# Optimization experiments

Hardware: AMD Instinct MI355X
Metric: run time of the kernel (lower is better)

Reference implementation:

```python
import jax, jax.numpy as jnp
import numpy as np

G, P, F, K = 256, 512, 4, 6   # graphs, nodes/graph, features, knn k
N = G * P

def _prelu(x, a):
    return jnp.where(x >= 0, x, a * x)

def _knn_edges(x):
    # per-graph brute-force kNN (k=6, no self loops), flow source->target
    xg = x.reshape(G, P, F)
    sq = jnp.sum(xg * xg, -1)                                   # [G,P]
    d = sq[:, :, None] + sq[:, None, :] - 2.0 * jnp.einsum('gpf,gqf->gpq', xg, xg)
    d = d + jnp.eye(P, dtype=x.dtype) * 1e10                    # exclude self
    _, idx = jax.lax.top_k(-d, K)                               # [G,P,K] neighbors
    off = (jnp.arange(G) * P)[:, None, None]
    src = (idx + off).reshape(-1)                               # message sources
    tgt = jnp.broadcast_to(jnp.arange(N).reshape(G, P, 1), (G, P, K)).reshape(-1)
    return src, tgt

def setup_inputs():
    key = jax.random.key(0)
    ks = jax.random.split(key, 8)
    f = lambda k, s: jax.random.normal(k, s, jnp.float32) * 0.1
    return {
        "x": jax.random.normal(ks[0], (N, F), jnp.float32),
        "batch": jnp.arange(N, dtype=jnp.int32) // P,
        "pre_W1": f(ks[1], (F, F)), "pre_b1": jnp.zeros((F,), jnp.float32),
        "pre_a1": jnp.full((F,), 0.25, jnp.float32),
        "pre_W2": f(ks[2], (F, F)), "pre_b2": jnp.zeros((F,), jnp.float32),
        "pre_a2": jnp.full((F,), 0.25, jnp.float32),
        "bn_g": jnp.ones((F,), jnp.float32), "bn_b": jnp.zeros((F,), jnp.float32),
        "act_a": jnp.full((F,), 0.25, jnp.float32),
        "conv_Wm": f(ks[3], (4, F, F)), "conv_bm": jnp.zeros((4, F), jnp.float32),
        "hlv_W1": f(ks[4], (5 * F, 5 * F)), "hlv_b1": jnp.zeros((5 * F,), jnp.float32),
        "hlv_W2": f(ks[5], (5 * F, 1)), "hlv_b2": jnp.zeros((1,), jnp.float32),
    }

def reference(x, batch, pre_W1, pre_b1, pre_a1, pre_W2, pre_b2, pre_a2,
              bn_g, bn_b, act_a, conv_Wm, conv_bm, hlv_W1, hlv_b1, hlv_W2, hlv_b2):
    src, tgt = _knn_edges(x)                                    # knn on raw x
    # pre_nn: Linear-PReLU-Linear-PReLU-BatchNorm (batch stats, training mode)
    h = _prelu(x @ pre_W1 + pre_b1, pre_a1)
    h = _prelu(h @ pre_W2 + pre_b2, pre_a2)
    mu = jnp.mean(h, 0)
    var = jnp.var(h, 0)
    h = (h - mu) / jnp.sqrt(var + 1e-5) * bn_g + bn_b
    xs = [h]
    for i in range(4):
        # GeneralConv (PyG defaults): sum-aggregate lin_msg(x_j) + identity skip
        msg = h[src] @ conv_Wm[i] + conv_bm[i]                  # [E,F]
        aggr = jax.ops.segment_sum(msg, tgt, num_segments=N)    # [N,F]
        h = _prelu(aggr + h, act_a)                             # shared PReLU act
        xs.append(h)
    hc = jnp.concatenate(xs, axis=-1)                           # JK 'cat' -> [N,5F]
    pooled = jax.ops.segment_sum(hc, batch, num_segments=G)     # global_add_pool
    out = jax.nn.relu(pooled @ hlv_W1 + hlv_b1) @ hlv_W2 + hlv_b2
    return out
```

## Files before the change

### kernel.cpp

```cpp
#include <hip/hip_runtime.h>

#define GG 256
#define PP 512
#define FF 4
#define KK 6
#define NN (GG*PP)

__device__ __forceinline__ unsigned umin_(unsigned a, unsigned b){ return a<b?a:b; }
__device__ __forceinline__ unsigned umax_(unsigned a, unsigned b){ return a>b?a:b; }
__device__ __forceinline__ float finf(){ return __int_as_float(0x7f800000); }

__device__ __forceinline__ unsigned mmap32(float d){
    int bb = __float_as_int(d);
    int t = bb >> 31;
    return (unsigned)(bb ^ (t | (int)0x80000000));
}

__device__ __forceinline__ void cas6_u64(uint64_t (&B)[6], uint64_t kv)
{
    bool c1 = kv < B[1]; bool c2 = kv < B[2]; bool c3 = kv < B[3];
    bool c4 = kv < B[4]; bool c5 = kv < B[5];
    B[0] = c1 ? B[1] : kv;
    B[1] = c2 ? B[2] : (c1 ? kv : B[1]);
    B[2] = c3 ? B[3] : (c2 ? kv : B[2]);
    B[3] = c4 ? B[4] : (c3 ? kv : B[3]);
    B[4] = c5 ? B[5] : (c4 ? kv : B[4]);
    B[5] = c5 ? kv : B[5];
}

#define INS7U(v){                                  \
    unsigned n0=umin_(M0,(v));                     \
    unsigned n1=umin_(M1,umax_((v),M0));           \
    unsigned n2=umin_(M2,umax_((v),M1));           \
    unsigned n3=umin_(M3,umax_((v),M2));           \
    unsigned n4=umin_(M4,umax_((v),M3));           \
    unsigned n5=umin_(M5,umax_((v),M4));           \
    unsigned n6=umin_(M6,umax_((v),M5));           \
    M0=n0;M1=n1;M2=n2;M3=n3;M4=n4;M5=n5;M6=n6; }

__global__ __launch_bounds__(512) void scan_kernel(
    const float* __restrict__ x,
    const float* __restrict__ pre_W1, const float* __restrict__ pre_b1, const float* __restrict__ pre_a1,
    const float* __restrict__ pre_W2, const float* __restrict__ pre_b2, const float* __restrict__ pre_a2,
    float* __restrict__ bn_part,
    int* __restrict__ knn_idx)
{
    __shared__ float4   xm2s[PP];
    __shared__ float    sqs[PP];
    __shared__ unsigned gmp[128][17];
    __shared__ float    Tv[128];
    __shared__ ushort   hits[128*50];
    __shared__ unsigned cnt4[128][4];
    __shared__ float    wred[8][8];

    const int t = threadIdx.x;
    const int bid = blockIdx.x;
    const int g = bid >> 2, quarter = bid & 3;
    const int gbase = g * PP;
    const int w = t >> 6, lane = t & 63;
    const int s  = w & 3;
    const int lt = (w >> 2)*64 + lane;
    const int p  = quarter*128 + lt;

    float4 xt = ((const float4*)x)[gbase + t];
    xm2s[t] = make_float4(-2.0f*xt.x, -2.0f*xt.y, -2.0f*xt.z, -2.0f*xt.w);
    sqs[t]  = xt.x*xt.x + xt.y*xt.y + xt.z*xt.z + xt.w*xt.w;

    if (quarter == 0){
        float h1[FF], h2[FF];
#pragma unroll
        for (int fo=0;fo<FF;fo++){
            float m = xt.x*pre_W1[0*FF+fo] + xt.y*pre_W1[1*FF+fo]
                    + xt.z*pre_W1[2*FF+fo] + xt.w*pre_W1[3*FF+fo] + pre_b1[fo];
            h1[fo] = m >= 0.0f ? m : pre_a1[fo]*m;
        }
#pragma unroll
        for (int fo=0;fo<FF;fo++){
            float m = h1[0]*pre_W2[0*FF+fo] + h1[1]*pre_W2[1*FF+fo]
                    + h1[2]*pre_W2[2*FF+fo] + h1[3]*pre_W2[3*FF+fo] + pre_b2[fo];
            h2[fo] = m >= 0.0f ? m : pre_a2[fo]*m;
        }
        float v[8];
#pragma unroll
        for (int f=0;f<4;f++){ v[f]=h2[f]; v[4+f]=h2[f]*h2[f]; }
#pragma unroll
        for (int off=32; off; off>>=1){
#pragma unroll
            for (int f=0;f<8;f++) v[f] += __shfl_down(v[f], off);
        }
        if ((t&63)==0){
#pragma unroll
            for (int f=0;f<8;f++) wred[w][f]=v[f];
        }
    }
    __syncthreads();
    if (quarter == 0 && t < 8){
        float a=0;
#pragma unroll
        for (int w2=0;w2<8;w2++) a += wred[w2][t];
        bn_part[t*GG + g] = a;
    }

    const int su = __builtin_amdgcn_readfirstlane(s);
    const int qb = su*128;

    const float4 xmv = xm2s[p];
    const float4 xp = make_float4(-0.5f*xmv.x, -0.5f*xmv.y, -0.5f*xmv.z, -0.5f*xmv.w);
    const float INF = finf();

#pragma unroll 1
    for (int gp2=0; gp2<4; gp2++){
        unsigned packed = 0;
#pragma unroll
        for (int sub=0; sub<2; sub++){
            const int base = qb + (gp2*2+sub)*16;
            float gm = INF;
#pragma unroll
            for (int pj=0; pj<8; pj++){
                const int q0 = base + pj*2;
                float4 a = xm2s[q0], b = xm2s[q0+1];
                float2 sq = *(const float2*)&sqs[q0];
                float da = fmaf(a.x,xp.x, fmaf(a.y,xp.y, fmaf(a.z,xp.z, fmaf(a.w,xp.w, sq.x))));
                float db = fmaf(b.x,xp.x, fmaf(b.y,xp.y, fmaf(b.z,xp.z, fmaf(b.w,xp.w, sq.y))));
                gm = fminf(gm, fminf(da, db));
            }
            unsigned u = mmap32(gm);
            unsigned r = (u >> 16) + ((u & 0xFFFFu) ? 1u : 0u);
            r = umin_(r, 0xFFFFu);
            packed |= r << (16*sub);
        }
        gmp[lt][su*4 + gp2] = packed;
    }
    __syncthreads();

    if (t < 128){
        unsigned M0=~0u,M1=~0u,M2=~0u,M3=~0u,M4=~0u,M5=~0u,M6=~0u;
#pragma unroll
        for (int j=0;j<16;j++){
            unsigned pr = gmp[t][j];
            unsigned v0 = pr & 0xFFFFu, v1 = pr >> 16;
            INS7U(v0); INS7U(v1);
        }
        unsigned Tcmp = M6 << 16;
        Tv[t] = (Tcmp & 0x80000000u) ? __uint_as_float(Tcmp ^ 0x80000000u)
                                     : __uint_as_float(~Tcmp);
    }
    __syncthreads();

    {
        const float Tf = Tv[lt];
        unsigned c = 0;
        ushort* hrow = &hits[lt*50 + su*12];
#pragma unroll 2
        for (int j=0;j<64;j++){
            const int q0 = qb + 2*j;
            float4 a = xm2s[q0], b = xm2s[q0+1];
            float2 sq = *(const float2*)&sqs[q0];
            float da = fmaf(a.x,xp.x, fmaf(a.y,xp.y, fmaf(a.z,xp.z, fmaf(a.w,xp.w, sq.x))));
            float db = fmaf(b.x,xp.x, fmaf(b.y,xp.y, fmaf(b.z,xp.z, fmaf(b.w,xp.w, sq.y))));
            bool hA = (da <= Tf), hB = (db <= Tf);
            if (hA || hB){
                int i0 = hA ? q0 : (q0+1);
                hrow[umin_(c,11u)] = (ushort)i0; c++;
                if (hA && hB){ hrow[umin_(c,11u)] = (ushort)(q0+1); c++; }
            }
        }
        cnt4[lt][su] = c;
    }
    __syncthreads();

    if (t < 128){
        uint4 cc = *(const uint4*)&cnt4[t][0];
        const int pt = quarter*128 + t;
        bool ovf = (cc.x>12u)||(cc.y>12u)||(cc.z>12u)||(cc.w>12u);
        float4 xmq = xm2s[pt];
        float4 xq = make_float4(-0.5f*xmq.x, -0.5f*xmq.y, -0.5f*xmq.z, -0.5f*xmq.w);
        uint64_t B[6];
#pragma unroll
        for (int j2=0;j2<6;j2++) B[j2] = ~0ull;
        if (!ovf){
#pragma unroll
            for (int s2=0;s2<4;s2++){
                unsigned cs = (s2==0)?cc.x:(s2==1)?cc.y:(s2==2)?cc.z:cc.w;
                const ushort* hr = &hits[t*50 + s2*12];
                for (unsigned j2=0;j2<cs;j2++){
                    int idx = hr[j2];
                    float4 a = xm2s[idx];
                    float d = fmaf(a.x,xq.x, fmaf(a.y,xq.y, fmaf(a.z,xq.z, fmaf(a.w,xq.w, sqs[idx]))));
                    uint64_t key = ((uint64_t)mmap32(d) << 32) | (unsigned)idx;
                    if (idx == pt) key = ~0ull;
                    if (key < B[0]) cas6_u64(B, key);
                }
            }
        } else {
            for (int q=0;q<PP;q++){
                float4 a = xm2s[q];
                float d = fmaf(a.x,xq.x, fmaf(a.y,xq.y, fmaf(a.z,xq.z, fmaf(a.w,xq.w, sqs[q]))));
                uint64_t key = ((uint64_t)mmap32(d) << 32) | (unsigned)q;
                if (q == pt) key = ~0ull;
                if (key < B[0]) cas6_u64(B, key);
            }
        }
#pragma unroll
        for (int j2=0;j2<6;j2++)
            knn_idx[j2*NN + gbase + pt] = (int)(B[j2] & 0xFFFFFFFFull);
    }
}

__global__ __launch_bounds__(512) void graph_kernel(
    const float* __restrict__ x,
    const int* __restrict__ knn_idx,
    const float* __restrict__ bn_part,
    const float* __restrict__ pre_W1, const float* __restrict__ pre_b1, const float* __restrict__ pre_a1,
    const float* __restrict__ pre_W2, const float* __restrict__ pre_b2, const float* __restrict__ pre_a2,
    const float* __restrict__ bn_g, const float* __restrict__ bn_b,
    const float* __restrict__ act_a,
    const float* __restrict__ conv_Wm, const float* __restrict__ conv_bm,
    const float* __restrict__ hlv_W1, const float* __restrict__ hlv_b1,
    const float* __restrict__ hlv_W2, const float* __restrict__ hlv_b2,
    float* __restrict__ out)
{
    __shared__ float4 hbuf[PP];
    __shared__ float wred[8][4];
    __shared__ float pooled[20];
    __shared__ float stats[8];
    __shared__ float hid[20];
    const int g = blockIdx.x, p = threadIdx.x;
    const int gp = g*PP + p;

    if (p < 64){
        int vv = p>>3, j = p&7;
        float acc = 0.0f;
        for (int i=j;i<GG;i+=8) acc += bn_part[vv*GG + i];
        acc += __shfl_xor(acc,1); acc += __shfl_xor(acc,2); acc += __shfl_xor(acc,4);
        if (j==0) stats[vv] = acc;
    }
    __syncthreads();
    if (p < 4){
        float mu  = stats[p]   * (1.0f/NN);
        float var = stats[4+p] * (1.0f/NN) - mu*mu;
        stats[p]   = mu;
        stats[4+p] = 1.0f / sqrtf(var + 1e-5f);
    }

    float4 xt = ((const float4*)x)[gp];
    float h1[FF], h2[FF];
#pragma unroll
    for (int fo=0;fo<FF;fo++){
        float m = xt.x*pre_W1[0*FF+fo] + xt.y*pre_W1[1*FF+fo]
                + xt.z*pre_W1[2*FF+fo] + xt.w*pre_W1[3*FF+fo] + pre_b1[fo];
        h1[fo] = m >= 0.0f ? m : pre_a1[fo]*m;
    }
#pragma unroll
    for (int fo=0;fo<FF;fo++){
        float m = h1[0]*pre_W2[0*FF+fo] + h1[1]*pre_W2[1*FF+fo]
                + h1[2]*pre_W2[2*FF+fo] + h1[3]*pre_W2[3*FF+fo] + pre_b2[fo];
        h2[fo] = m >= 0.0f ? m : pre_a2[fo]*m;
    }
    __syncthreads();

    float hp[4];
#pragma unroll
    for (int f=0;f<4;f++)
        hp[f] = (h2[f] - stats[f]) * stats[4+f] * bn_g[f] + bn_b[f];
    hbuf[p] = make_float4(hp[0],hp[1],hp[2],hp[3]);
    int nb[KK];
#pragma unroll
    for (int j=0;j<KK;j++) nb[j] = knn_idx[j*NN + gp];

    auto block_accum = [&](const float* h, int slice){
        float v0=h[0], v1=h[1], v2=h[2], v3=h[3];
#pragma unroll
        for (int off=32; off; off>>=1){
            v0 += __shfl_down(v0,off); v1 += __shfl_down(v1,off);
            v2 += __shfl_down(v2,off); v3 += __shfl_down(v3,off);
        }
        int w = p>>6;
        if ((p&63)==0){ wred[w][0]=v0; wred[w][1]=v1; wred[w][2]=v2; wred[w][3]=v3; }
        __syncthreads();
        if (p < 4){
            float a=0;
#pragma unroll
            for (int w2=0;w2<8;w2++) a += wred[w2][p];
            pooled[slice*4+p] = a;
        }
        __syncthreads();
    };

    block_accum(hp, 0);

#pragma unroll 1
    for (int L=0; L<4; L++){
        float4 sm = make_float4(0.f,0.f,0.f,0.f);
#pragma unroll
        for (int j=0;j<KK;j++){
            float4 hn = hbuf[nb[j]];
            sm.x+=hn.x; sm.y+=hn.y; sm.z+=hn.z; sm.w+=hn.w;
        }
        const float* W  = conv_Wm + L*16;
        const float* bm = conv_bm + L*4;
        float nh[4];
#pragma unroll
        for (int fo=0;fo<4;fo++){
            float m = sm.x*W[0*4+fo] + sm.y*W[1*4+fo] + sm.z*W[2*4+fo] + sm.w*W[3*4+fo]
                    + 6.0f*bm[fo] + hp[fo];
            float a = act_a[fo];
            nh[fo] = m >= 0.0f ? m : a*m;
        }
        __syncthreads();
        hbuf[p] = make_float4(nh[0],nh[1],nh[2],nh[3]);
#pragma unroll
        for (int f=0;f<4;f++) hp[f]=nh[f];
        block_accum(hp, L+1);
    }

    if (p < 20){
        float acc = hlv_b1[p];
#pragma unroll 1
        for (int k2=0;k2<20;k2++) acc += pooled[k2]*hlv_W1[k2*20+p];
        hid[p] = acc > 0.0f ? acc : 0.0f;
    }
    __syncthreads();
    if (p == 0){
        float o = hlv_b2[0];
#pragma unroll 1
        for (int j=0;j<20;j++) o += hid[j]*hlv_W2[j];
        out[g] = o;
    }
}

extern "C" void kernel_launch(void* const* d_in, const int* in_sizes, int n_in,
                              void* d_out, int out_size, void* d_ws, size_t ws_size,
                              hipStream_t stream)
{
    const float* x      = (const float*)d_in[0];
    const float* pre_W1 = (const float*)d_in[2];
    const float* pre_b1 = (const float*)d_in[3];
    const float* pre_a1 = (const float*)d_in[4];
    const float* pre_W2 = (const float*)d_in[5];
    const float* pre_b2 = (const float*)d_in[6];
    const float* pre_a2 = (const float*)d_in[7];
    const float* bn_g   = (const float*)d_in[8];
    const float* bn_b   = (const float*)d_in[9];
    const float* act_a  = (const float*)d_in[10];
    const float* conv_Wm= (const float*)d_in[11];
    const float* conv_bm= (const float*)d_in[12];
    const float* hlv_W1 = (const float*)d_in[13];
    const float* hlv_b1 = (const float*)d_in[14];
    const float* hlv_W2 = (const float*)d_in[15];
    const float* hlv_b2 = (const float*)d_in[16];

    char* ws = (char*)d_ws;
    int*   knn     = (int*)ws;
    float* bn_part = (float*)(ws + (size_t)6*NN*sizeof(int));

    scan_kernel<<<GG*4, PP, 0, stream>>>(x, pre_W1,pre_b1,pre_a1,
                                         pre_W2,pre_b2,pre_a2, bn_part, knn);
    graph_kernel<<<GG, PP, 0, stream>>>(x, knn, bn_part,
                                        pre_W1,pre_b1,pre_a1, pre_W2,pre_b2,pre_a2,
                                        bn_g,bn_b, act_a, conv_Wm,conv_bm,
                                        hlv_W1,hlv_b1,hlv_W2,hlv_b2,
                                        (float*)d_out);
}
```

Baseline: 64.51 us.

## Process one graph per block with register-tiled 8-query scan and hit bitmasks

The kNN scan now runs one block per graph instead of four. Each wave owns a 64-candidate slice and computes distances for 8 query points per lane, so every candidate loaded from LDS is reused across 8 queries. Candidate hits are recorded as 32-bit bitmasks rather than capped per-query index lists, which removes the overflow fallback path that scanned all candidates. The trade-offs are a quarter of the blocks (less parallelism across CUs), more LDS and registers per block, and a serial clz loop over the bitmask set bits in the final selection.

```diff
diff --git a/kernel.cpp b/kernel.cpp
--- a/kernel.cpp
+++ b/kernel.cpp
@@ -47,26 +47,22 @@
 {
     __shared__ float4   xm2s[PP];
     __shared__ float    sqs[PP];
-    __shared__ unsigned gmp[128][17];
-    __shared__ float    Tv[128];
-    __shared__ ushort   hits[128*50];
-    __shared__ unsigned cnt4[128][4];
+    __shared__ ushort   gmp16[32][PP];
+    __shared__ float    Tv[PP];
+    __shared__ unsigned mbuf[16][PP];
     __shared__ float    wred[8][8];
 
     const int t = threadIdx.x;
-    const int bid = blockIdx.x;
-    const int g = bid >> 2, quarter = bid & 3;
+    const int g = blockIdx.x;
     const int gbase = g * PP;
     const int w = t >> 6, lane = t & 63;
-    const int s  = w & 3;
-    const int lt = (w >> 2)*64 + lane;
-    const int p  = quarter*128 + lt;
+    const int wu = __builtin_amdgcn_readfirstlane(w);
+    const int qb = wu * 64;
 
     float4 xt = ((const float4*)x)[gbase + t];
     xm2s[t] = make_float4(-2.0f*xt.x, -2.0f*xt.y, -2.0f*xt.z, -2.0f*xt.w);
     sqs[t]  = xt.x*xt.x + xt.y*xt.y + xt.z*xt.z + xt.w*xt.w;
-
-    if (quarter == 0){
+    {
         float h1[FF], h2[FF];
 #pragma unroll
         for (int fo=0;fo<FF;fo++){
@@ -88,122 +84,118 @@
 #pragma unroll
             for (int f=0;f<8;f++) v[f] += __shfl_down(v[f], off);
         }
-        if ((t&63)==0){
+        if (lane==0){
 #pragma unroll
             for (int f=0;f<8;f++) wred[w][f]=v[f];
         }
     }
     __syncthreads();
-    if (quarter == 0 && t < 8){
+    if (t < 8){
         float a=0;
 #pragma unroll
         for (int w2=0;w2<8;w2++) a += wred[w2][t];
         bn_part[t*GG + g] = a;
     }
 
-    const int su = __builtin_amdgcn_readfirstlane(s);
-    const int qb = su*128;
-
-    const float4 xmv = xm2s[p];
-    const float4 xp = make_float4(-0.5f*xmv.x, -0.5f*xmv.y, -0.5f*xmv.z, -0.5f*xmv.w);
+    float4 xp[8];
+#pragma unroll
+    for (int j=0;j<8;j++){
+        float4 v = xm2s[lane + 64*j];
+        xp[j] = make_float4(-0.5f*v.x, -0.5f*v.y, -0.5f*v.z, -0.5f*v.w);
+    }
     const float INF = finf();
 
 #pragma unroll 1
-    for (int gp2=0; gp2<4; gp2++){
-        unsigned packed = 0;
-#pragma unroll
-        for (int sub=0; sub<2; sub++){
-            const int base = qb + (gp2*2+sub)*16;
-            float gm = INF;
-#pragma unroll
-            for (int pj=0; pj<8; pj++){
-                const int q0 = base + pj*2;
-                float4 a = xm2s[q0], b = xm2s[q0+1];
-                float2 sq = *(const float2*)&sqs[q0];
-                float da = fmaf(a.x,xp.x, fmaf(a.y,xp.y, fmaf(a.z,xp.z, fmaf(a.w,xp.w, sq.x))));
-                float db = fmaf(b.x,xp.x, fmaf(b.y,xp.y, fmaf(b.z,xp.z, fmaf(b.w,xp.w, sq.y))));
-                gm = fminf(gm, fminf(da, db));
+    for (int grp=0; grp<4; grp++){
+        float gm[8];
+#pragma unroll
+        for (int j=0;j<8;j++) gm[j]=INF;
+#pragma unroll
+        for (int i2=0;i2<8;i2++){
+            const int q0 = qb + grp*16 + i2*2;
+            float4 a = xm2s[q0], b = xm2s[q0+1];
+            float2 sq = *(const float2*)&sqs[q0];
+#pragma unroll
+            for (int j=0;j<8;j++){
+                float da = fmaf(a.x,xp[j].x, fmaf(a.y,xp[j].y, fmaf(a.z,xp[j].z, fmaf(a.w,xp[j].w, sq.x))));
+                float db = fmaf(b.x,xp[j].x, fmaf(b.y,xp[j].y, fmaf(b.z,xp[j].z, fmaf(b.w,xp[j].w, sq.y))));
+                gm[j] = fminf(gm[j], fminf(da, db));
             }
-            unsigned u = mmap32(gm);
+        }
+#pragma unroll
+        for (int j=0;j<8;j++){
+            unsigned u = mmap32(gm[j]);
             unsigned r = (u >> 16) + ((u & 0xFFFFu) ? 1u : 0u);
             r = umin_(r, 0xFFFFu);
-            packed |= r << (16*sub);
-        }
-        gmp[lt][su*4 + gp2] = packed;
-    }
-    __syncthreads();
-
-    if (t < 128){
+            gmp16[wu*4 + grp][lane + 64*j] = (ushort)r;
+        }
+    }
+    __syncthreads();
+
+    {
         unsigned M0=~0u,M1=~0u,M2=~0u,M3=~0u,M4=~0u,M5=~0u,M6=~0u;
 #pragma unroll
-        for (int j=0;j<16;j++){
-            unsigned pr = gmp[t][j];
-            unsigned v0 = pr & 0xFFFFu, v1 = pr >> 16;
-            INS7U(v0); INS7U(v1);
-        }
-        unsigned Tcmp = M6 << 16;
-        Tv[t] = (Tcmp & 0x80000000u) ? __uint_as_float(Tcmp ^ 0x80000000u)
-                                     : __uint_as_float(~Tcmp);
-    }
-    __syncthreads();
-
-    {
-        const float Tf = Tv[lt];
-        unsigned c = 0;
-        ushort* hrow = &hits[lt*50 + su*12];
-#pragma unroll 2
-        for (int j=0;j<64;j++){
-            const int q0 = qb + 2*j;
+        for (int r=0;r<32;r++){
+            unsigned v = gmp16[r][t];
+            INS7U(v);
+        }
+        unsigned Tc = M6 << 16;
+        Tv[t] = (Tc & 0x80000000u) ? __uint_as_float(Tc ^ 0x80000000u)
+                                   : __uint_as_float(~Tc);
+    }
+    __syncthreads();
+
+    float Tf[8];
+#pragma unroll
+    for (int j=0;j<8;j++) Tf[j] = Tv[lane + 64*j];
+
+#pragma unroll 1
+    for (int h=0; h<2; h++){
+        unsigned m[8];
+#pragma unroll
+        for (int j=0;j<8;j++) m[j]=0;
+#pragma unroll 4
+        for (int i2=0;i2<16;i2++){
+            const int q0 = qb + h*32 + i2*2;
             float4 a = xm2s[q0], b = xm2s[q0+1];
             float2 sq = *(const float2*)&sqs[q0];
-            float da = fmaf(a.x,xp.x, fmaf(a.y,xp.y, fmaf(a.z,xp.z, fmaf(a.w,xp.w, sq.x))));
-            float db = fmaf(b.x,xp.x, fmaf(b.y,xp.y, fmaf(b.z,xp.z, fmaf(b.w,xp.w, sq.y))));
-            bool hA = (da <= Tf), hB = (db <= Tf);
-            if (hA || hB){
-                int i0 = hA ? q0 : (q0+1);
-                hrow[umin_(c,11u)] = (ushort)i0; c++;
-                if (hA && hB){ hrow[umin_(c,11u)] = (ushort)(q0+1); c++; }
+#pragma unroll
+            for (int j=0;j<8;j++){
+                float da = fmaf(a.x,xp[j].x, fmaf(a.y,xp[j].y, fmaf(a.z,xp[j].z, fmaf(a.w,xp[j].w, sq.x))));
+                float db = fmaf(b.x,xp[j].x, fmaf(b.y,xp[j].y, fmaf(b.z,xp[j].z, fmaf(b.w,xp[j].w, sq.y))));
+                m[j] = m[j] + m[j] + (da <= Tf[j] ? 1u : 0u);
+                m[j] = m[j] + m[j] + (db <= Tf[j] ? 1u : 0u);
             }
         }
-        cnt4[lt][su] = c;
-    }
-    __syncthreads();
-
-    if (t < 128){
-        uint4 cc = *(const uint4*)&cnt4[t][0];
-        const int pt = quarter*128 + t;
-        bool ovf = (cc.x>12u)||(cc.y>12u)||(cc.z>12u)||(cc.w>12u);
-        float4 xmq = xm2s[pt];
+#pragma unroll
+        for (int j=0;j<8;j++) mbuf[wu*2 + h][lane + 64*j] = m[j];
+    }
+    __syncthreads();
+
+    {
+        float4 xmq = xm2s[t];
         float4 xq = make_float4(-0.5f*xmq.x, -0.5f*xmq.y, -0.5f*xmq.z, -0.5f*xmq.w);
         uint64_t B[6];
 #pragma unroll
         for (int j2=0;j2<6;j2++) B[j2] = ~0ull;
-        if (!ovf){
-#pragma unroll
-            for (int s2=0;s2<4;s2++){
-                unsigned cs = (s2==0)?cc.x:(s2==1)?cc.y:(s2==2)?cc.z:cc.w;
-                const ushort* hr = &hits[t*50 + s2*12];
-                for (unsigned j2=0;j2<cs;j2++){
-                    int idx = hr[j2];
-                    float4 a = xm2s[idx];
-                    float d = fmaf(a.x,xq.x, fmaf(a.y,xq.y, fmaf(a.z,xq.z, fmaf(a.w,xq.w, sqs[idx]))));
-                    uint64_t key = ((uint64_t)mmap32(d) << 32) | (unsigned)idx;
-                    if (idx == pt) key = ~0ull;
-                    if (key < B[0]) cas6_u64(B, key);
-                }
-            }
-        } else {
-            for (int q=0;q<PP;q++){
-                float4 a = xm2s[q];
-                float d = fmaf(a.x,xq.x, fmaf(a.y,xq.y, fmaf(a.z,xq.z, fmaf(a.w,xq.w, sqs[q]))));
-                uint64_t key = ((uint64_t)mmap32(d) << 32) | (unsigned)q;
-                if (q == pt) key = ~0ull;
+#pragma unroll 1
+        for (int r=0;r<16;r++){
+            unsigned m = mbuf[r][t];
+            const int base = (r>>1)*64 + (r&1)*32;
+            while (m){
+                int c = __builtin_clz(m);
+                m &= ~(0x80000000u >> c);
+                int idx = base + c;
+                float4 a = xm2s[idx];
+                float d = fmaf(a.x,xq.x, fmaf(a.y,xq.y, fmaf(a.z,xq.z, fmaf(a.w,xq.w, sqs[idx]))));
+                uint64_t key = ((uint64_t)mmap32(d) << 32) | (unsigned)idx;
+                if (idx == t) key = ~0ull;
                 if (key < B[0]) cas6_u64(B, key);
             }
         }
 #pragma unroll
         for (int j2=0;j2<6;j2++)
-            knn_idx[j2*NN + gbase + pt] = (int)(B[j2] & 0xFFFFFFFFull);
+            knn_idx[j2*NN + gbase + t] = (int)(B[j2] & 0xFFFFFFFFull);
     }
 }
 
@@ -354,8 +346,8 @@
     int*   knn     = (int*)ws;
     float* bn_part = (float*)(ws + (size_t)6*NN*sizeof(int));
 
-    scan_kernel<<<GG*4, PP, 0, stream>>>(x, pre_W1,pre_b1,pre_a1,
-                                         pre_W2,pre_b2,pre_a2, bn_part, knn);
+    scan_kernel<<<GG, PP, 0, stream>>>(x, pre_W1,pre_b1,pre_a1,
+                                       pre_W2,pre_b2,pre_a2, bn_part, knn);
     graph_kernel<<<GG, PP, 0, stream>>>(x, knn, bn_part,
                                         pre_W1,pre_b1,pre_a1, pre_W2,pre_b2,pre_a2,
                                         bn_g,bn_b, act_a, conv_Wm,conv_bm,
```

Result: faster. 57.08 us (-11.5%).
